# Kernel tuning notes

Hardware: AMD Instinct MI355X
Metric: run time of the kernel (lower is better)

## Reference

```python
import jax, jax.numpy as jnp
import numpy as np

N = 50000      # nodes
E = 800000     # edges
F_IN = 128     # n_features
H = 4          # n_heads
C1 = 64        # n_hidden (per-head out of layer 1)
C2 = 32        # n_classes (per-head out of layer 2)
NEG_SLOPE = 0.2
EPS = 1e-16


def setup_inputs() -> dict:
    key = jax.random.key(0)
    ks = jax.random.split(key, 12)
    x = jax.random.normal(ks[0], (N, F_IN), dtype=jnp.float32)
    edge_index = jax.random.randint(ks[1], (2, E), 0, N, dtype=jnp.int64)
    # layer 1 params (GATConv: shared lin for src/dst, att_src/att_dst vectors, bias)
    W1 = jax.random.normal(ks[2], (F_IN, H * C1), dtype=jnp.float32) * (1.0 / np.sqrt(F_IN))
    att_src1 = jax.random.normal(ks[3], (H, C1), dtype=jnp.float32) * 0.1
    att_dst1 = jax.random.normal(ks[4], (H, C1), dtype=jnp.float32) * 0.1
    b1 = jnp.zeros((C1,), dtype=jnp.float32)
    # layer 2 params
    W2 = jax.random.normal(ks[5], (C1, H * C2), dtype=jnp.float32) * (1.0 / np.sqrt(C1))
    att_src2 = jax.random.normal(ks[6], (H, C2), dtype=jnp.float32) * 0.1
    att_dst2 = jax.random.normal(ks[7], (H, C2), dtype=jnp.float32) * 0.1
    b2 = jnp.zeros((C2,), dtype=jnp.float32)
    return {"x": x, "edge_index": edge_index,
            "W1": W1, "att_src1": att_src1, "att_dst1": att_dst1, "b1": b1,
            "W2": W2, "att_src2": att_src2, "att_dst2": att_dst2, "b2": b2}


def gat_conv(x, src, dst, W, att_src, att_dst, b, heads, out_ch):
    """PyG GATConv with concat=False (head-averaged output)."""
    n = x.shape[0]
    h = (x @ W).reshape(n, heads, out_ch)                 # [N, H, C]
    a_s = jnp.einsum('nhc,hc->nh', h, att_src)            # [N, H]
    a_d = jnp.einsum('nhc,hc->nh', h, att_dst)            # [N, H]
    e = jax.nn.leaky_relu(a_s[src] + a_d[dst], NEG_SLOPE)  # [E, H]
    # segment softmax over edges grouped by destination node
    m = jax.ops.segment_max(e, dst, num_segments=n)        # [N, H]
    m = jnp.where(jnp.isfinite(m), m, 0.0)
    ex = jnp.exp(e - m[dst])                               # [E, H]
    denom = jax.ops.segment_sum(ex, dst, num_segments=n)   # [N, H]
    alpha = ex / (denom[dst] + EPS)                        # [E, H]
    # scatter-add aggregation of attended source features
    msg = alpha[:, :, None] * h[src]                       # [E, H, C]
    out = jax.ops.segment_sum(msg, dst, num_segments=n)    # [N, H, C]
    return out.mean(axis=1) + b                            # [N, C]


def reference(x, edge_index, W1, att_src1, att_dst1, b1, W2, att_src2, att_dst2, b2):
    src, dst = edge_index[0], edge_index[1]
    h = jax.nn.relu(gat_conv(x, src, dst, W1, att_src1, att_dst1, b1, H, C1))
    # dropout is identity in eval mode
    out = gat_conv(h, src, dst, W2, att_src2, att_dst2, b2, H, C2)
    return out
```

## Files before the change

### kernel.cpp

```cpp
#include <hip/hip_runtime.h>
#include <hip/hip_fp16.h>
#include <cstdint>
#include <cstddef>

#define N_NODES 50000
#define N_EDGES 800000
#define F_IN 128
#define H_HEADS 4
#define C1 64
#define C2 32
#define NEG_SLOPE 0.2f
#define EPS_GAT 1e-16f

typedef _Float16 half8 __attribute__((ext_vector_type(8)));
typedef float f32x4 __attribute__((ext_vector_type(4)));

template<int K, int M>
__device__ __forceinline__ void wtrans_dev(const float* __restrict__ W,
                                           _Float16* __restrict__ Wt,
                                           _Float16* tile, int bm, int bk) {
    const int m0 = bm * 64, k0 = bk * 64;
    const int t = threadIdx.x;
    const int c = t & 63;
#pragma unroll
    for (int j = 0; j < 16; ++j) {
        int r = (t >> 6) + 4 * j;
        tile[c * 66 + r] = (_Float16)W[(size_t)(k0 + r) * M + m0 + c];
    }
    __syncthreads();
#pragma unroll
    for (int j = 0; j < 16; ++j) {
        int m_l = (t >> 6) + 4 * j;
        Wt[(size_t)(m0 + m_l) * K + k0 + c] = tile[m_l * 66 + c];
    }
}

__global__ __launch_bounds__(256) void wtrans_both_kernel(
        const float* __restrict__ W1, _Float16* __restrict__ wt1,
        const float* __restrict__ W2, _Float16* __restrict__ wt2) {
    __shared__ _Float16 tile[64 * 66];
    int b = blockIdx.x;
    if (b < 8) {
        wtrans_dev<F_IN, H_HEADS * C1>(W1, wt1, tile, b & 3, b >> 2);
    } else {
        wtrans_dev<C1, H_HEADS * C2>(W2, wt2, tile, b - 8, 0);
    }
}

template<int K, int M, int Hn, int C, typename InT>
__global__ __launch_bounds__(256) void gemm_att_kernel(
        const InT* __restrict__ X, const _Float16* __restrict__ Wt,
        _Float16* __restrict__ Hout,
        const float* __restrict__ atts, const float* __restrict__ attd,
        float* __restrict__ as_, float* __restrict__ ad_, int Nr) {
    constexpr int LDK = K + 8;
    constexpr int NCT = M / 64;
    constexpr int HPB = 64 / C;
    __shared__ _Float16 Ah[64 * LDK];
    __shared__ _Float16 Bt[64 * LDK];
    __shared__ _Float16 Ht[64 * 72];
    const int row0 = blockIdx.x * 64;
    const int t = threadIdx.x;
    const int wv = t >> 6;
    const int lane = t & 63;
    const int quad = lane >> 4;
    const int n16 = lane & 15;

    if constexpr (sizeof(InT) == 4) {
        constexpr int KQ = K / 4;
#pragma unroll
        for (int j = 0; j < (64 * KQ) / 256; ++j) {
            int flat = t + 256 * j;
            int r = flat / KQ, kq = flat % KQ;
            int rg = row0 + r;
            float4 v = make_float4(0.f, 0.f, 0.f, 0.f);
            if (rg < Nr) v = *(const float4*)&X[(size_t)rg * K + 4 * kq];
            _Float16 tmp[4] = {(_Float16)v.x, (_Float16)v.y, (_Float16)v.z, (_Float16)v.w};
            *(uint2*)&Ah[r * LDK + 4 * kq] = *(const uint2*)tmp;
        }
    } else {
        constexpr int KQ = K / 8;
#pragma unroll
        for (int j = 0; j < (64 * KQ) / 256; ++j) {
            int flat = t + 256 * j;
            int r = flat / KQ, kq = flat % KQ;
            int rg = row0 + r;
            uint4 v = make_uint4(0u, 0u, 0u, 0u);
            if (rg < Nr) v = *(const uint4*)&X[(size_t)rg * K + 8 * kq];
            *(uint4*)&Ah[r * LDK + 8 * kq] = v;
        }
    }
    __syncthreads();

    half8 af[K / 32];
    const _Float16* Ap = &Ah[(16 * wv + n16) * LDK + 8 * quad];
#pragma unroll
    for (int ki = 0; ki < K / 32; ++ki) af[ki] = *(const half8*)(Ap + 32 * ki);

    for (int ct = 0; ct < NCT; ++ct) {
        const int col0 = 64 * ct;
        __syncthreads();
        {
            constexpr int KQ8 = K / 8;
#pragma unroll
            for (int j = 0; j < (64 * KQ8) / 256; ++j) {
                int flat = t + 256 * j;
                int c = flat / KQ8, kq = flat % KQ8;
                uint4 v = *(const uint4*)&Wt[(size_t)(col0 + c) * K + 8 * kq];
                *(uint4*)&Bt[c * LDK + 8 * kq] = v;
            }
        }
        __syncthreads();

        f32x4 acc[4];
#pragma unroll
        for (int nf = 0; nf < 4; ++nf) acc[nf] = (f32x4){0.f, 0.f, 0.f, 0.f};
#pragma unroll
        for (int ki = 0; ki < K / 32; ++ki) {
#pragma unroll
            for (int nf = 0; nf < 4; ++nf) {
                half8 bf = *(const half8*)&Bt[(16 * nf + n16) * LDK + 32 * ki + 8 * quad];
                acc[nf] = __builtin_amdgcn_mfma_f32_16x16x32_f16(af[ki], bf, acc[nf], 0, 0, 0);
            }
        }

        float dps[HPB][4], dpd[HPB][4];
#pragma unroll
        for (int u = 0; u < HPB; ++u)
#pragma unroll
            for (int r = 0; r < 4; ++r) { dps[u][r] = 0.f; dpd[u][r] = 0.f; }
#pragma unroll
        for (int nf = 0; nf < 4; ++nf) {
            int gc = col0 + 16 * nf + n16;
            float cs = atts[gc], cd = attd[gc];
#pragma unroll
            for (int r = 0; r < 4; ++r) {
                float av = acc[nf][r];
                dps[(16 * nf) / C][r] += av * cs;
                dpd[(16 * nf) / C][r] += av * cd;
            }
        }
#pragma unroll
        for (int u = 0; u < HPB; ++u)
#pragma unroll
            for (int r = 0; r < 4; ++r) {
                float s = dps[u][r], d = dpd[u][r];
#pragma unroll
                for (int off = 1; off < 16; off <<= 1) {
                    s += __shfl_xor(s, off, 64);
                    d += __shfl_xor(d, off, 64);
                }
                dps[u][r] = s; dpd[u][r] = d;
            }
        if (n16 == 0) {
            const int h0 = col0 / C;
#pragma unroll
            for (int r = 0; r < 4; ++r) {
                int row = row0 + 16 * wv + 4 * quad + r;
                if (row < Nr) {
#pragma unroll
                    for (int u = 0; u < HPB; ++u) {
                        as_[row * Hn + h0 + u] = dps[u][r];
                        ad_[row * Hn + h0 + u] = dpd[u][r];
                    }
                }
            }
        }

#pragma unroll
        for (int nf = 0; nf < 4; ++nf)
#pragma unroll
            for (int r = 0; r < 4; ++r)
                Ht[(16 * wv + 4 * quad + r) * 72 + 16 * nf + n16] = (_Float16)acc[nf][r];
        __syncthreads();
#pragma unroll
        for (int j = 0; j < 2; ++j) {
            int chunk = t + 256 * j;
            int r = chunk >> 3, cc = chunk & 7;
            int row = row0 + r;
            if (row < Nr) {
                uint4 v = *(const uint4*)&Ht[r * 72 + 8 * cc];
                *(uint4*)&Hout[(size_t)row * M + col0 + 8 * cc] = v;
            }
        }
    }
}

__global__ __launch_bounds__(256) void count_kernel(const int* __restrict__ dst,
                                                    int* __restrict__ deg, int Ecnt) {
    int e = blockIdx.x * 256 + threadIdx.x;
    if (e < Ecnt) atomicAdd(&deg[dst[e]], 1);
}

__global__ __launch_bounds__(256) void scan_partial(const int* __restrict__ deg,
                                                    int* __restrict__ bsum, int n) {
    int i = blockIdx.x * 256 + threadIdx.x;
    int v = (i < n) ? deg[i] : 0;
    int lane = threadIdx.x & 63, wv = threadIdx.x >> 6;
#pragma unroll
    for (int off = 32; off > 0; off >>= 1) v += __shfl_down(v, off, 64);
    __shared__ int wt[4];
    if (lane == 0) wt[wv] = v;
    __syncthreads();
    if (threadIdx.x == 0) bsum[blockIdx.x] = wt[0] + wt[1] + wt[2] + wt[3];
}

__global__ __launch_bounds__(256) void scan_base(int* __restrict__ bsum, int nb,
                                                 int* __restrict__ total_out) {
    int t = threadIdx.x, lane = t & 63, wv = t >> 6;
    int v = (t < nb) ? bsum[t] : 0;
    int x = v;
#pragma unroll
    for (int off = 1; off < 64; off <<= 1) {
        int y = __shfl_up(x, off, 64);
        if (lane >= off) x += y;
    }
    __shared__ int wt[4];
    if (lane == 63) wt[wv] = x;
    __syncthreads();
    int base = 0;
    for (int k = 0; k < wv; ++k) base += wt[k];
    if (t < nb) bsum[t] = base + x - v;
    if (t == 255) *total_out = base + x;
}

__global__ __launch_bounds__(256) void scan_final(const int* __restrict__ deg,
                                                  const int* __restrict__ bsum,
                                                  int* __restrict__ row_off,
                                                  int* __restrict__ cursor, int n) {
    int i = blockIdx.x * 256 + threadIdx.x;
    int t = threadIdx.x, lane = t & 63, wv = t >> 6;
    int v = (i < n) ? deg[i] : 0;
    int x = v;
#pragma unroll
    for (int off = 1; off < 64; off <<= 1) {
        int y = __shfl_up(x, off, 64);
        if (lane >= off) x += y;
    }
    __shared__ int wt[4];
    if (lane == 63) wt[wv] = x;
    __syncthreads();
    int base = bsum[blockIdx.x];
    for (int k = 0; k < wv; ++k) base += wt[k];
    int ro = base + x - v;
    if (i < n) { row_off[i] = ro; cursor[i] = ro; }
}

__global__ __launch_bounds__(256) void scatter_kernel(const int* __restrict__ src,
                                                      const int* __restrict__ dst,
                                                      int* __restrict__ cursor,
                                                      unsigned short* __restrict__ ssrc,
                                                      int Ecnt) {
    int e = blockIdx.x * 256 + threadIdx.x;
    if (e >= Ecnt) return;
    int p = atomicAdd(&cursor[dst[e]], 1);
    ssrc[p] = (unsigned short)src[e];
}

template<int Hn, int C, bool RELU, bool OUT_F16>
__global__ __launch_bounds__(256) void gat_agg_kernel(
        const int* __restrict__ row_off, const unsigned short* __restrict__ ssrc,
        const float* __restrict__ as_, const float* __restrict__ ad_,
        const _Float16* __restrict__ Hm, const float* __restrict__ bias,
        void* __restrict__ outv, int Nr) {
    constexpr int HC = Hn * C;
    constexpr int PER = HC / 16;
    constexpr int NV = PER / 8;
    int node = blockIdx.x * 4 + (threadIdx.x >> 6);
    int lane = threadIdx.x & 63;
    if (node >= Nr) return;
    const int g = lane >> 4;
    const int l = lane & 15;
    const int h = l >> 2;
    const float ad_h = ad_[node * Hn + h];

    const int begin = row_off[node], end = row_off[node + 1];
    const int iters = (end - begin + 3) >> 2;

    float acc[PER];
#pragma unroll
    for (int t = 0; t < PER; ++t) acc[t] = 0.f;
    float wsum = 0.f;

    int idx = begin + g;
    int s_cur = (idx < end) ? (int)ssrc[idx] : -1;
    int s_nx = (idx + 4 < end) ? (int)ssrc[idx + 4] : -1;
    float a_cur = 0.f;
    uint4 u_cur[NV] = {};
    if (s_cur >= 0) {
        a_cur = as_[s_cur * Hn + h];
        const uint4* hp = (const uint4*)(Hm + (size_t)s_cur * HC + l * PER);
        u_cur[0] = hp[0];
        if constexpr (NV == 2) u_cur[1] = hp[1];
    }

    for (int it = 0; it < iters; ++it) {
        const int s_pf = s_nx;
        s_nx = (idx + 8 < end) ? (int)ssrc[idx + 8] : -1;
        float a_nx = 0.f;
        uint4 u_nx[NV] = {};
        if (s_pf >= 0) {
            a_nx = as_[s_pf * Hn + h];
            const uint4* hp = (const uint4*)(Hm + (size_t)s_pf * HC + l * PER);
            u_nx[0] = hp[0];
            if constexpr (NV == 2) u_nx[1] = hp[1];
        }
        float logit = a_cur + ad_h;
        logit = (logit > 0.f) ? logit : NEG_SLOPE * logit;
        float w = (s_cur >= 0) ? __expf(logit) : 0.f;
        wsum += w;
#pragma unroll
        for (int v = 0; v < NV; ++v) {
            float2 f;
            f = __half22float2(*(const __half2*)&u_cur[v].x);
            acc[8 * v + 0] += w * f.x; acc[8 * v + 1] += w * f.y;
            f = __half22float2(*(const __half2*)&u_cur[v].y);
            acc[8 * v + 2] += w * f.x; acc[8 * v + 3] += w * f.y;
            f = __half22float2(*(const __half2*)&u_cur[v].z);
            acc[8 * v + 4] += w * f.x; acc[8 * v + 5] += w * f.y;
            f = __half22float2(*(const __half2*)&u_cur[v].w);
            acc[8 * v + 6] += w * f.x; acc[8 * v + 7] += w * f.y;
        }
        s_cur = s_pf; a_cur = a_nx;
#pragma unroll
        for (int v = 0; v < NV; ++v) u_cur[v] = u_nx[v];
        idx += 4;
    }

#pragma unroll
    for (int t = 0; t < PER; ++t) {
        acc[t] += __shfl_xor(acc[t], 16, 64);
        acc[t] += __shfl_xor(acc[t], 32, 64);
    }
    wsum += __shfl_xor(wsum, 16, 64);
    wsum += __shfl_xor(wsum, 32, 64);
    const float inv = 1.f / (wsum + EPS_GAT);
    float val[PER];
#pragma unroll
    for (int t = 0; t < PER; ++t) {
        float v = acc[t] * inv;
        v += __shfl_xor(v, 4, 64);
        v += __shfl_xor(v, 8, 64);
        val[t] = v * (1.0f / Hn);
    }
    if (lane < 4) {
        const int c0 = lane * PER;
#pragma unroll
        for (int t = 0; t < PER; ++t) {
            float v = val[t] + bias[c0 + t];
            if (RELU) v = fmaxf(v, 0.f);
            val[t] = v;
        }
        if constexpr (OUT_F16) {
            _Float16* o = (_Float16*)outv;
            _Float16 tmp[PER];
#pragma unroll
            for (int t = 0; t < PER; ++t) tmp[t] = (_Float16)val[t];
            uint4* d4 = (uint4*)&o[(size_t)node * C + c0];
            d4[0] = *(const uint4*)&tmp[0];
            if constexpr (NV == 2) d4[1] = *(const uint4*)&tmp[8];
        } else {
            float* o = (float*)outv;
#pragma unroll
            for (int t4 = 0; t4 < PER / 4; ++t4)
                *(float4*)&o[(size_t)node * C + c0 + 4 * t4] =
                    make_float4(val[4 * t4 + 0], val[4 * t4 + 1],
                                val[4 * t4 + 2], val[4 * t4 + 3]);
        }
    }
}

extern "C" void kernel_launch(void* const* d_in, const int* in_sizes, int n_in,
                              void* d_out, int out_size, void* d_ws, size_t ws_size,
                              hipStream_t stream) {
    const float* x    = (const float*)d_in[0];
    const int*   ei   = (const int*)d_in[1];
    const float* W1   = (const float*)d_in[2];
    const float* as1w = (const float*)d_in[3];
    const float* ad1w = (const float*)d_in[4];
    const float* b1   = (const float*)d_in[5];
    const float* W2   = (const float*)d_in[6];
    const float* as2w = (const float*)d_in[7];
    const float* ad2w = (const float*)d_in[8];
    const float* b2   = (const float*)d_in[9];
    float* out = (float*)d_out;

    const int* src = ei;
    const int* dst = ei + N_EDGES;

    char* ws = (char*)d_ws;
    size_t off = 0;
    auto alloc = [&](size_t bytes) -> void* {
        void* p = ws + off;
        off = (off + bytes + 255) & ~(size_t)255;
        return p;
    };
    const int NB = (N_NODES + 255) / 256;
    int*   deg  = (int*)alloc((size_t)N_NODES * 4);
    float* as1_ = (float*)alloc((size_t)N_NODES * H_HEADS * 4);
    float* ad1_ = (float*)alloc((size_t)N_NODES * H_HEADS * 4);
    float* as2_ = (float*)alloc((size_t)N_NODES * H_HEADS * 4);
    float* ad2_ = (float*)alloc((size_t)N_NODES * H_HEADS * 4);

    _Float16* h1   = (_Float16*)alloc((size_t)N_NODES * H_HEADS * C1 * 2);
    _Float16* out1 = (_Float16*)alloc((size_t)N_NODES * C1 * 2);
    _Float16* h2   = (_Float16*)alloc((size_t)N_NODES * H_HEADS * C2 * 2);
    _Float16* wt1  = (_Float16*)alloc((size_t)(H_HEADS * C1) * F_IN * 2);
    _Float16* wt2  = (_Float16*)alloc((size_t)(H_HEADS * C2) * C1 * 2);
    int*   row_off = (int*)alloc((size_t)(N_NODES + 1) * 4);
    int*   cursor  = (int*)alloc((size_t)N_NODES * 4);
    unsigned short* ssrc = (unsigned short*)alloc((size_t)N_EDGES * 2);
    int*   bsum    = (int*)alloc((size_t)NB * 4);

    hipMemsetAsync(deg, 0, (size_t)N_NODES * 4, stream);
    wtrans_both_kernel<<<10, 256, 0, stream>>>(W1, wt1, W2, wt2);
    count_kernel<<<(N_EDGES + 255) / 256, 256, 0, stream>>>(dst, deg, N_EDGES);
    scan_partial<<<NB, 256, 0, stream>>>(deg, bsum, N_NODES);
    scan_base<<<1, 256, 0, stream>>>(bsum, NB, &row_off[N_NODES]);
    scan_final<<<NB, 256, 0, stream>>>(deg, bsum, row_off, cursor, N_NODES);
    scatter_kernel<<<(N_EDGES + 255) / 256, 256, 0, stream>>>(src, dst, cursor, ssrc, N_EDGES);

    gemm_att_kernel<F_IN, H_HEADS * C1, H_HEADS, C1, float>
        <<<(N_NODES + 63) / 64, 256, 0, stream>>>(
            x, wt1, h1, as1w, ad1w, as1_, ad1_, N_NODES);
    gat_agg_kernel<H_HEADS, C1, true, true><<<(N_NODES + 3) / 4, 256, 0, stream>>>(
        row_off, ssrc, as1_, ad1_, h1, b1, (void*)out1, N_NODES);

    gemm_att_kernel<C1, H_HEADS * C2, H_HEADS, C2, _Float16>
        <<<(N_NODES + 63) / 64, 256, 0, stream>>>(
            out1, wt2, h2, as2w, ad2w, as2_, ad2_, N_NODES);
    gat_agg_kernel<H_HEADS, C2, false, false><<<(N_NODES + 3) / 4, 256, 0, stream>>>(
        row_off, ssrc, as2_, ad2_, h2, b2, (void*)out, N_NODES);
}
```

Measured before the change: 294.5 us.

## Fuse CSR build and weight transpose into one cooperative kernel

Replaces the memset, weight-transpose, degree count, three-phase scan and scatter launches with a single cooperative kernel of 512 blocks that uses grid-wide syncs between phases. The goal is to remove the per-launch overhead and idle gaps of six small dependent launches. In exchange, grid.sync barriers cost time and only 512 blocks run the edge loops, which can lower atomic throughput compared with the original 3125-block launches.

Measured after the change: 590.3 us. 100% more time.

```diff
diff --git a/kernel.cpp b/kernel.cpp
--- a/kernel.cpp
+++ b/kernel.cpp
@@ -1,7 +1,10 @@
 #include <hip/hip_runtime.h>
 #include <hip/hip_fp16.h>
+#include <hip/hip_cooperative_groups.h>
 #include <cstdint>
 #include <cstddef>
+
+namespace cg = cooperative_groups;
 
 #define N_NODES 50000
 #define N_EDGES 800000
@@ -12,6 +15,9 @@
 #define NEG_SLOPE 0.2f
 #define EPS_GAT 1e-16f
 
+#define PREP_BLOCKS 512
+#define PREP_CHUNK ((N_NODES + PREP_BLOCKS - 1) / PREP_BLOCKS)
+
 typedef _Float16 half8 __attribute__((ext_vector_type(8)));
 typedef float f32x4 __attribute__((ext_vector_type(4)));
 
@@ -35,15 +41,93 @@
     }
 }
 
-__global__ __launch_bounds__(256) void wtrans_both_kernel(
-        const float* __restrict__ W1, _Float16* __restrict__ wt1,
-        const float* __restrict__ W2, _Float16* __restrict__ wt2) {
+struct PrepArgs {
+    const int* src; const int* dst;
+    int* deg; int* bsum; int* row_off; int* cursor;
+    unsigned short* ssrc;
+    const float* W1; _Float16* wt1;
+    const float* W2; _Float16* wt2;
+};
+
+__global__ __launch_bounds__(256) void prep_kernel(PrepArgs a) {
+    cg::grid_group grid = cg::this_grid();
+    const int t = threadIdx.x;
+    const int b = blockIdx.x;
+    const int lane = t & 63, wv = t >> 6;
     __shared__ _Float16 tile[64 * 66];
-    int b = blockIdx.x;
+    __shared__ int wsum_s[4];
+
+    for (int i = b * 256 + t; i < N_NODES; i += PREP_BLOCKS * 256) a.deg[i] = 0;
     if (b < 8) {
-        wtrans_dev<F_IN, H_HEADS * C1>(W1, wt1, tile, b & 3, b >> 2);
-    } else {
-        wtrans_dev<C1, H_HEADS * C2>(W2, wt2, tile, b - 8, 0);
+        wtrans_dev<F_IN, H_HEADS * C1>(a.W1, a.wt1, tile, b & 3, b >> 2);
+    } else if (b < 10) {
+        wtrans_dev<C1, H_HEADS * C2>(a.W2, a.wt2, tile, b - 8, 0);
+    }
+    grid.sync();
+
+    for (int e = b * 256 + t; e < N_EDGES; e += PREP_BLOCKS * 256)
+        atomicAdd(&a.deg[a.dst[e]], 1);
+    grid.sync();
+
+    {
+        const int base = b * PREP_CHUNK;
+        const int lim = N_NODES - base;
+        int v = (t < lim && t < PREP_CHUNK) ? a.deg[base + t] : 0;
+#pragma unroll
+        for (int off = 32; off > 0; off >>= 1) v += __shfl_down(v, off, 64);
+        if (lane == 0) wsum_s[wv] = v;
+        __syncthreads();
+        if (t == 0) a.bsum[b] = wsum_s[0] + wsum_s[1] + wsum_s[2] + wsum_s[3];
+    }
+    grid.sync();
+
+    if (b == 0) {
+        int v0 = a.bsum[2 * t], v1 = a.bsum[2 * t + 1];
+        int s = v0 + v1;
+        int x = s;
+#pragma unroll
+        for (int off = 1; off < 64; off <<= 1) {
+            int y = __shfl_up(x, off, 64);
+            if (lane >= off) x += y;
+        }
+        __syncthreads();
+        if (lane == 63) wsum_s[wv] = x;
+        __syncthreads();
+        int woff = 0;
+        for (int k = 0; k < wv; ++k) woff += wsum_s[k];
+        int excl = woff + x - s;
+        a.bsum[2 * t]     = excl;
+        a.bsum[2 * t + 1] = excl + v0;
+        if (t == 255) a.row_off[N_NODES] = woff + x;
+    }
+    grid.sync();
+
+    {
+        const int base = b * PREP_CHUNK;
+        const int lim = N_NODES - base;
+        int v = (t < lim && t < PREP_CHUNK) ? a.deg[base + t] : 0;
+        int x = v;
+#pragma unroll
+        for (int off = 1; off < 64; off <<= 1) {
+            int y = __shfl_up(x, off, 64);
+            if (lane >= off) x += y;
+        }
+        __syncthreads();
+        if (lane == 63) wsum_s[wv] = x;
+        __syncthreads();
+        int woff = a.bsum[b];
+        for (int k = 0; k < wv; ++k) woff += wsum_s[k];
+        int excl = woff + x - v;
+        if (t < lim && t < PREP_CHUNK) {
+            a.row_off[base + t] = excl;
+            a.cursor[base + t] = excl;
+        }
+    }
+    grid.sync();
+
+    for (int e = b * 256 + t; e < N_EDGES; e += PREP_BLOCKS * 256) {
+        int p = atomicAdd(&a.cursor[a.dst[e]], 1);
+        a.ssrc[p] = (unsigned short)a.src[e];
     }
 }
 
@@ -186,77 +270,6 @@
     }
 }
 
-__global__ __launch_bounds__(256) void count_kernel(const int* __restrict__ dst,
-                                                    int* __restrict__ deg, int Ecnt) {
-    int e = blockIdx.x * 256 + threadIdx.x;
-    if (e < Ecnt) atomicAdd(&deg[dst[e]], 1);
-}
-
-__global__ __launch_bounds__(256) void scan_partial(const int* __restrict__ deg,
-                                                    int* __restrict__ bsum, int n) {
-    int i = blockIdx.x * 256 + threadIdx.x;
-    int v = (i < n) ? deg[i] : 0;
-    int lane = threadIdx.x & 63, wv = threadIdx.x >> 6;
-#pragma unroll
-    for (int off = 32; off > 0; off >>= 1) v += __shfl_down(v, off, 64);
-    __shared__ int wt[4];
-    if (lane == 0) wt[wv] = v;
-    __syncthreads();
-    if (threadIdx.x == 0) bsum[blockIdx.x] = wt[0] + wt[1] + wt[2] + wt[3];
-}
-
-__global__ __launch_bounds__(256) void scan_base(int* __restrict__ bsum, int nb,
-                                                 int* __restrict__ total_out) {
-    int t = threadIdx.x, lane = t & 63, wv = t >> 6;
-    int v = (t < nb) ? bsum[t] : 0;
-    int x = v;
-#pragma unroll
-    for (int off = 1; off < 64; off <<= 1) {
-        int y = __shfl_up(x, off, 64);
-        if (lane >= off) x += y;
-    }
-    __shared__ int wt[4];
-    if (lane == 63) wt[wv] = x;
-    __syncthreads();
-    int base = 0;
-    for (int k = 0; k < wv; ++k) base += wt[k];
-    if (t < nb) bsum[t] = base + x - v;
-    if (t == 255) *total_out = base + x;
-}
-
-__global__ __launch_bounds__(256) void scan_final(const int* __restrict__ deg,
-                                                  const int* __restrict__ bsum,
-                                                  int* __restrict__ row_off,
-                                                  int* __restrict__ cursor, int n) {
-    int i = blockIdx.x * 256 + threadIdx.x;
-    int t = threadIdx.x, lane = t & 63, wv = t >> 6;
-    int v = (i < n) ? deg[i] : 0;
-    int x = v;
-#pragma unroll
-    for (int off = 1; off < 64; off <<= 1) {
-        int y = __shfl_up(x, off, 64);
-        if (lane >= off) x += y;
-    }
-    __shared__ int wt[4];
-    if (lane == 63) wt[wv] = x;
-    __syncthreads();
-    int base = bsum[blockIdx.x];
-    for (int k = 0; k < wv; ++k) base += wt[k];
-    int ro = base + x - v;
-    if (i < n) { row_off[i] = ro; cursor[i] = ro; }
-}
-
-__global__ __launch_bounds__(256) void scatter_kernel(const int* __restrict__ src,
-                                                      const int* __restrict__ dst,
-                                                      int* __restrict__ cursor,
-                                                      unsigned short* __restrict__ ssrc,
-                                                      int Ecnt) {
-    int e = blockIdx.x * 256 + threadIdx.x;
-    if (e >= Ecnt) return;
-    int p = atomicAdd(&cursor[dst[e]], 1);
-    ssrc[p] = (unsigned short)src[e];
-}
-
 template<int Hn, int C, bool RELU, bool OUT_F16>
 __global__ __launch_bounds__(256) void gat_agg_kernel(
         const int* __restrict__ row_off, const unsigned short* __restrict__ ssrc,
@@ -395,7 +408,6 @@
         off = (off + bytes + 255) & ~(size_t)255;
         return p;
     };
-    const int NB = (N_NODES + 255) / 256;
     int*   deg  = (int*)alloc((size_t)N_NODES * 4);
     float* as1_ = (float*)alloc((size_t)N_NODES * H_HEADS * 4);
     float* ad1_ = (float*)alloc((size_t)N_NODES * H_HEADS * 4);
@@ -410,15 +422,16 @@
     int*   row_off = (int*)alloc((size_t)(N_NODES + 1) * 4);
     int*   cursor  = (int*)alloc((size_t)N_NODES * 4);
     unsigned short* ssrc = (unsigned short*)alloc((size_t)N_EDGES * 2);
-    int*   bsum    = (int*)alloc((size_t)NB * 4);
-
-    hipMemsetAsync(deg, 0, (size_t)N_NODES * 4, stream);
-    wtrans_both_kernel<<<10, 256, 0, stream>>>(W1, wt1, W2, wt2);
-    count_kernel<<<(N_EDGES + 255) / 256, 256, 0, stream>>>(dst, deg, N_EDGES);
-    scan_partial<<<NB, 256, 0, stream>>>(deg, bsum, N_NODES);
-    scan_base<<<1, 256, 0, stream>>>(bsum, NB, &row_off[N_NODES]);
-    scan_final<<<NB, 256, 0, stream>>>(deg, bsum, row_off, cursor, N_NODES);
-    scatter_kernel<<<(N_EDGES + 255) / 256, 256, 0, stream>>>(src, dst, cursor, ssrc, N_EDGES);
+    int*   bsum    = (int*)alloc((size_t)PREP_BLOCKS * 4);
+
+    PrepArgs pa;
+    pa.src = src; pa.dst = dst;
+    pa.deg = deg; pa.bsum = bsum; pa.row_off = row_off; pa.cursor = cursor;
+    pa.ssrc = ssrc;
+    pa.W1 = W1; pa.wt1 = wt1; pa.W2 = W2; pa.wt2 = wt2;
+    void* kargs[] = { &pa };
+    hipLaunchCooperativeKernel((const void*)prep_kernel,
+                               dim3(PREP_BLOCKS), dim3(256), kargs, 0, stream);
 
     gemm_att_kernel<F_IN, H_HEADS * C1, H_HEADS, C1, float>
         <<<(N_NODES + 63) / 64, 256, 0, stream>>>(
```
